# Performance work log

Hardware: AMD Instinct MI355X
Metric: run time of the kernel (lower is better)

## Reference

```python
import jax, jax.numpy as jnp
import numpy as np

VOCAB, E, H, L, B, OUT = 50000, 300, 300, 75, 2048, 5

def setup_inputs() -> dict:
    key = jax.random.key(0)
    ks = jax.random.split(key, 12)
    s_e = 1.0 / np.sqrt(E)
    s_h = 1.0 / np.sqrt(H)
    return {
        "input_sequences": jax.random.randint(ks[0], (B, L), 0, VOCAB),
        "emb": jax.random.normal(ks[1], (VOCAB, E), jnp.float32) * 0.1,
        "W_ih": jax.random.normal(ks[2], (3 * H, E), jnp.float32) * s_e,
        "W_hh": jax.random.normal(ks[3], (3 * H, H), jnp.float32) * s_h,
        "b_ih": jax.random.normal(ks[4], (3 * H,), jnp.float32) * s_h,
        "b_hh": jax.random.normal(ks[5], (3 * H,), jnp.float32) * s_h,
        "wCo_w": jax.random.normal(ks[6], (3 * H,), jnp.float32) * (1.0 / np.sqrt(3 * H)),
        "wCo_b": jax.random.normal(ks[7], (1,), jnp.float32) * 0.02,
        "Wmy_w": jax.random.normal(ks[8], (L,), jnp.float32) * (1.0 / np.sqrt(L)),
        "Wmy_b": jax.random.normal(ks[9], (1,), jnp.float32) * 0.02,
        "logits_w": jax.random.normal(ks[10], (OUT, H), jnp.float32) * s_h,
        "logits_b": jax.random.normal(ks[11], (OUT,), jnp.float32) * 0.02,
    }

def _gru(x_tm, W_ih, W_hh, b_ih, b_hh):
    # x_tm: (L, B, E) time-major. PyTorch GRU cell math.
    gx_all = jnp.einsum("lbe,ge->lbg", x_tm, W_ih) + b_ih  # (L, B, 3H)
    h0 = jnp.zeros((x_tm.shape[1], W_hh.shape[1]), x_tm.dtype)
    def step(h, gx):
        gh = h @ W_hh.T + b_hh
        xr, xz, xn = jnp.split(gx, 3, axis=-1)
        hr, hz, hn = jnp.split(gh, 3, axis=-1)
        r = jax.nn.sigmoid(xr + hr)
        z = jax.nn.sigmoid(xz + hz)
        n = jnp.tanh(xn + r * hn)
        h_new = (1.0 - z) * n + z * h
        return h_new, h_new
    _, ys = jax.lax.scan(step, h0, gx_all)
    return ys  # (L, B, H)

def reference(input_sequences, emb, W_ih, W_hh, b_ih, b_hh,
              wCo_w, wCo_b, Wmy_w, Wmy_b, logits_w, logits_b):
    x = emb[input_sequences]                      # (B, L, E)
    out_tm = _gru(x.transpose(1, 0, 2), W_ih, W_hh, b_ih, b_hh)  # (L, B, H)
    h = out_tm.transpose(1, 0, 2)                 # (B, L, H)
    # co_attention: s_ij = wCo @ cat(h_i, h_j, h_i*h_j) + b
    # computed WITHOUT materializing the (B, L, L, 3H) tensor:
    wa, wb, wc = jnp.split(wCo_w, 3)
    a = h @ wa                                    # (B, L)
    b = h @ wb                                    # (B, L)
    c = jnp.einsum("bid,bjd->bij", h * wc, h)     # (B, L, L)
    s = a[:, :, None] + b[:, None, :] + c + wCo_b[0]
    # zero the diagonal (mask = ones - diag)
    s = s * (1.0 - jnp.eye(s.shape[1], dtype=s.dtype))
    # Wmy: Linear(75, 1) over the j axis
    sm = s @ Wmy_w + Wmy_b[0]                     # (B, L)
    attn = jax.nn.softmax(sm, axis=1)             # softmax over i
    pooled = jnp.einsum("bi,bih->bh", attn, h)    # (B, H)
    return pooled @ logits_w.T + logits_b         # (B, OUT)
```

## Files before the change

kernel.cpp:

```cpp
#include <hip/hip_runtime.h>
#include <stdint.h>


typedef float f32x4 __attribute__((ext_vector_type(4)));
typedef short bf16x8 __attribute__((ext_vector_type(8)));
typedef _Float16 f16x4 __attribute__((ext_vector_type(4)));
typedef unsigned short u16;
typedef u16 u16x8 __attribute__((ext_vector_type(8)));
typedef u16 u16x4 __attribute__((ext_vector_type(4)));

#define DI __device__ __forceinline__

template <int N> struct IC { static constexpr int v = N; };

DI float bf2f(u16 v) {
    uint32_t u = ((uint32_t)v) << 16;
    float f;
    __builtin_memcpy(&f, &u, 4);
    return f;
}
DI u16 f2bf(float f) {
    uint32_t u;
    __builtin_memcpy(&u, &f, 4);
    uint32_t r = u + 0x7fffu + ((u >> 16) & 1u);
    return (u16)(r >> 16);
}
DI u16 cvt1(const void* p, int i, int f32m) {
    return f32m ? f2bf(((const float*)p)[i]) : ((const u16*)p)[i];
}

DI u16x8 load_row8(const u16* __restrict__ base, int e0) {
    u16x4 z = {0, 0, 0, 0};
    u16x4 lo = (e0 < 300) ? *(const u16x4*)(base + e0) : z;
    u16x4 hi = (e0 + 4 < 300) ? *(const u16x4*)(base + e0 + 4) : z;
    u16x8 r;
    r[0] = lo[0]; r[1] = lo[1]; r[2] = lo[2]; r[3] = lo[3];
    r[4] = hi[0]; r[5] = hi[1]; r[6] = hi[2]; r[7] = hi[3];
    return r;
}
DI u16x8 load_row8_f32(const float* __restrict__ base, int e0) {
    f32x4 z = {0.f, 0.f, 0.f, 0.f};
    f32x4 lo = (e0 < 300) ? *(const f32x4*)(base + e0) : z;
    f32x4 hi = (e0 + 4 < 300) ? *(const f32x4*)(base + e0 + 4) : z;
    u16x8 r;
    r[0] = f2bf(lo[0]); r[1] = f2bf(lo[1]); r[2] = f2bf(lo[2]); r[3] = f2bf(lo[3]);
    r[4] = f2bf(hi[0]); r[5] = f2bf(hi[1]); r[6] = f2bf(hi[2]); r[7] = f2bf(hi[3]);
    return r;
}

__global__ __launch_bounds__(256) void detect_dtype(const u16* __restrict__ raw,
                                                    int* __restrict__ flag) {
    __shared__ int cnt;
    if (threadIdx.x == 0) cnt = 0;
    __syncthreads();
    int local = 0;
    for (int i = threadIdx.x; i < 4096; i += 256) {
        int e = (raw[i] >> 7) & 0xFF;
        if (e >= 140) local++;
    }
    atomicAdd(&cnt, local);
    __syncthreads();
    if (threadIdx.x == 0) flag[0] = (cnt > 256) ? 1 : 0;
}

__global__ __launch_bounds__(256) void conv_big(const void* __restrict__ in,
                                                u16* __restrict__ outp, int n,
                                                const int* __restrict__ flag) {
    const int f32m = flag[0];
    int i0 = (blockIdx.x * 256 + threadIdx.x) * 8;
#pragma unroll
    for (int k = 0; k < 8; k++) {
        int i = i0 + k;
        if (i < n) outp[i] = cvt1(in, i, f32m);
    }
}

__global__ __launch_bounds__(256) void conv_smalls(
    const void* bih_r, const void* bhh_r, const void* wCo_r, const void* wCob_r,
    const void* Wmy_r, const void* Wmyb_r, const void* lw_r, const void* lb_r,
    u16* __restrict__ smalls, const int* __restrict__ flag) {
    const int f32m = flag[0];
    int t = blockIdx.x * 256 + threadIdx.x;
    if (t < 900) smalls[t] = cvt1(bih_r, t, f32m);
    else if (t < 1800) smalls[1024 + t - 900] = cvt1(bhh_r, t - 900, f32m);
    else if (t < 2700) smalls[2048 + t - 1800] = cvt1(wCo_r, t - 1800, f32m);
    else if (t < 2775) smalls[3072 + t - 2700] = cvt1(Wmy_r, t - 2700, f32m);
    else if (t < 4275) smalls[3200 + t - 2775] = cvt1(lw_r, t - 2775, f32m);
    else if (t < 4280) smalls[4704 + t - 4275] = cvt1(lb_r, t - 4275, f32m);
    else if (t == 4280) smalls[4712] = cvt1(wCob_r, 0, f32m);
    else if (t == 4281) smalls[4713] = cvt1(Wmyb_r, 0, f32m);
}

__global__ __launch_bounds__(256) void prep_img(const u16* __restrict__ W,
                                                u16* __restrict__ img) {
    int t = blockIdx.x * 256 + threadIdx.x;
    if (t >= 60 * 10 * 64) return;
    int lane = t & 63;
    int kt = (t >> 6) % 10;
    int nt = t / 640;
    int g = nt * 16 + (lane & 15);
    int gate = g / 320, u = g - gate * 320;
    int e0 = kt * 32 + (lane >> 4) * 8;
    u16x8 v;
    if (u < 300) {
        v = load_row8(W + (size_t)(gate * 300 + u) * 300, e0);
    } else {
        u16x8 z = {0, 0, 0, 0, 0, 0, 0, 0};
        v = z;
    }
    *(u16x8*)&img[(size_t)t * 8] = v;
}

__global__ __launch_bounds__(256) void zero_hstate(float* __restrict__ hs) {
    int t = blockIdx.x * 256 + threadIdx.x;
    f32x4 z = {0.f, 0.f, 0.f, 0.f};
    ((f32x4*)hs)[t] = z;
}

__global__ __launch_bounds__(256, 2) void gemm1_kernel(
    const int* __restrict__ seq, const void* __restrict__ emb_raw,
    const u16* __restrict__ Wimg, const u16* __restrict__ bih,
    _Float16* __restrict__ gxn, int ck, int phase, int BC, int bshift,
    const int* __restrict__ flag) {
    __shared__ int ids[192];
    __shared__ __align__(16) u16 Aimg[12 * 64 * 8];
    __shared__ __align__(16) u16 Bbuf[12 * 64 * 8];

    const int tid = threadIdx.x;
    const int lane = tid & 63, wv = tid >> 6, q = lane >> 4, c = lane & 15;
    const int m0 = blockIdx.x * 192;
    const int nb = blockIdx.y;
    const int f32m = flag[0];

    if (tid < 192) {
        int m = m0 + tid;
        int bc = m & (BC - 1);
        int tp = m >> bshift;
        ids[tid] = seq[(size_t)(phase * BC + bc) * 75 + ck * 15 + tp];
    }
    __syncthreads();

    f32x4 acc[3][12];
#pragma unroll
    for (int mt = 0; mt < 3; mt++)
#pragma unroll
        for (int nt = 0; nt < 12; nt++) {
            f32x4 z = {0.f, 0.f, 0.f, 0.f};
            acc[mt][nt] = z;
        }

    for (int kt = 0; kt < 10; kt++) {
#pragma unroll
        for (int s = 0; s < 3; s++) {
            int o = tid + s * 256;
            int qq = o / 192;
            int r = o - qq * 192;
            int e0 = kt * 32 + qq * 8;
            u16x8 v = f32m ? load_row8_f32((const float*)emb_raw + (size_t)ids[r] * 300, e0)
                           : load_row8((const u16*)emb_raw + (size_t)ids[r] * 300, e0);
            *(u16x8*)&Aimg[(((r >> 4) * 64) + ((r & 15) | (qq << 4))) * 8] = v;
        }
#pragma unroll
        for (int s = 0; s < 3; s++) {
            int ch = tid + s * 256;
            *(u16x8*)&Bbuf[ch * 8] =
                *(const u16x8*)&Wimg[(((size_t)(nb * 12 + (ch >> 6)) * 10 + kt) * 64 + (ch & 63)) * 8];
        }
        __syncthreads();

        bf16x8 a[3];
#pragma unroll
        for (int mt = 0; mt < 3; mt++) {
            u16x8 tmp = *(const u16x8*)&Aimg[(((wv * 3 + mt) * 64) + lane) * 8];
            a[mt] = __builtin_bit_cast(bf16x8, tmp);
        }
#pragma unroll
        for (int nt = 0; nt < 12; nt++) {
            u16x8 tb = *(const u16x8*)&Bbuf[(nt * 64 + lane) * 8];
            bf16x8 b = __builtin_bit_cast(bf16x8, tb);
#pragma unroll
            for (int mt = 0; mt < 3; mt++)
                acc[mt][nt] = __builtin_amdgcn_mfma_f32_16x16x32_bf16(a[mt], b, acc[mt][nt], 0, 0, 0);
        }
        __syncthreads();
    }

#pragma unroll
    for (int nt = 0; nt < 12; nt++) {
        int g = nb * 192 + nt * 16 + c;
        int gate = g / 320, u = g - gate * 320;
        float bias = (u < 300) ? bf2f(bih[gate * 300 + u]) : 0.f;
#pragma unroll
        for (int mt = 0; mt < 3; mt++) {
            int mrow = m0 + (wv * 3 + mt) * 16 + q * 4;
#pragma unroll
            for (int reg = 0; reg < 4; reg++) {
                gxn[((size_t)(mrow + reg) * 320 + u) * 4 + gate] =
                    (_Float16)(acc[mt][nt][reg] + bias);
            }
        }
    }
}

__global__ __launch_bounds__(512, 1) void gru_chunk(
    const _Float16* __restrict__ gxn, const u16* __restrict__ Wimg,
    const u16* __restrict__ bhh_g, u16* __restrict__ h_all,
    float* __restrict__ hstate, int ck, int BC) {
    __shared__ __align__(16) u16 Hhi[10 * 64 * 8];
    __shared__ __align__(16) u16 Hlo[10 * 64 * 8];
    __shared__ __align__(16) u16 Wlds[61440];

    const int tid = threadIdx.x;
    const int lane = tid & 63, wv = tid >> 6, q = lane >> 4, c = lane & 15;
    const int b0 = blockIdx.x * 16;
    const int wbase = (wv < 4) ? wv * 9216 : 36864 + (wv - 4) * 6144;

    float bhh[3][3];
    float hm[3][4];

    auto STAGE = [&](int kt, int buf, auto NTIC) {
        constexpr int NTI = NTIC.v;
        u16* dst = &Wlds[wbase + buf * (NTI * 3 * 512)];
#pragma unroll
        for (int Ti = 0; Ti < NTI; Ti++)
#pragma unroll
            for (int g = 0; g < 3; g++) {
                int nt = g * 20 + (wv + 8 * Ti);
                __builtin_amdgcn_global_load_lds(
                    (const unsigned int*)(Wimg + (size_t)(nt * 10 + kt) * 512 + lane * 8),
                    (unsigned int*)(dst + (Ti * 3 + g) * 512), 16, 0, 0);
            }
    };

    if (wv < 4) STAGE(0, 0, IC<3>{}); else STAGE(0, 0, IC<2>{});

    auto INIT = [&](auto NTIC) {
        constexpr int NTI = NTIC.v;
#pragma unroll
        for (int Ti = 0; Ti < NTI; Ti++) {
            int T = wv + 8 * Ti;
            int u = T * 16 + c;
#pragma unroll
            for (int g = 0; g < 3; g++)
                bhh[Ti][g] = (u < 300) ? bf2f(bhh_g[g * 300 + u]) : 0.f;
            int kti = T >> 1;
            int qp = ((T & 1) << 1) | (c >> 3);
            int j = c & 7;
#pragma unroll
            for (int reg = 0; reg < 4; reg++) {
                int m = q * 4 + reg;
                float h = hstate[(size_t)(b0 + m) * 320 + u];
                hm[Ti][reg] = h;
                int idx = (kti * 64 + ((q * 4 + reg) | (qp << 4))) * 8 + j;
                u16 hi = f2bf(h);
                Hhi[idx] = hi;
                Hlo[idx] = f2bf(h - bf2f(hi));
            }
        }
    };
    if (wv < 4) INIT(IC<3>{}); else INIT(IC<2>{});
    __syncthreads();

    for (int tt = 0; tt < 15; tt++) {
        auto PH1 = [&](auto NTIC) {
            constexpr int NTI = NTIC.v;
            constexpr int NT3 = NTI * 3;
            f16x4 gxv[NTI][4];
            const _Float16* gxt = gxn + (size_t)tt * BC * 1280;
#pragma unroll
            for (int Ti = 0; Ti < NTI; Ti++) {
                int u = (wv + 8 * Ti) * 16 + c;
#pragma unroll
                for (int reg = 0; reg < 4; reg++) {
                    int m = q * 4 + reg;
                    gxv[Ti][reg] = *(const f16x4*)&gxt[((size_t)(b0 + m) * 320 + u) * 4];
                }
            }

            f32x4 acc[NTI][3];
#pragma unroll
            for (int Ti = 0; Ti < NTI; Ti++)
#pragma unroll
                for (int g = 0; g < 3; g++) {
                    f32x4 z = {0.f, 0.f, 0.f, 0.f};
                    acc[Ti][g] = z;
                }

#pragma unroll 2
            for (int kt = 0; kt < 10; kt++) {
                if (kt < 9) STAGE(kt + 1, (kt + 1) & 1, NTIC);
                else if (tt < 14) STAGE(0, 0, NTIC);
                if (kt == 9 && tt == 14) {
                    asm volatile("s_waitcnt vmcnt(0)" ::: "memory");
                } else if constexpr (NTI == 3) {
                    asm volatile("s_waitcnt vmcnt(9)" ::: "memory");
                } else {
                    asm volatile("s_waitcnt vmcnt(6)" ::: "memory");
                }

                u16x8 th = *(const u16x8*)&Hhi[(kt * 64 + lane) * 8];
                u16x8 tl = *(const u16x8*)&Hlo[(kt * 64 + lane) * 8];
                bf16x8 ahi = __builtin_bit_cast(bf16x8, th);
                bf16x8 alo = __builtin_bit_cast(bf16x8, tl);
                const u16* wb = &Wlds[wbase + (kt & 1) * (NT3 * 512)];
#pragma unroll
                for (int Ti = 0; Ti < NTI; Ti++)
#pragma unroll
                    for (int g = 0; g < 3; g++) {
                        u16x8 tb = *(const u16x8*)&wb[(Ti * 3 + g) * 512 + lane * 8];
                        bf16x8 b = __builtin_bit_cast(bf16x8, tb);
                        acc[Ti][g] = __builtin_amdgcn_mfma_f32_16x16x32_bf16(
                            ahi, b, acc[Ti][g], 0, 0, 0);
                        acc[Ti][g] = __builtin_amdgcn_mfma_f32_16x16x32_bf16(
                            alo, b, acc[Ti][g], 0, 0, 0);
                    }
            }

            const int tglob = ck * 15 + tt;
#pragma unroll
            for (int Ti = 0; Ti < NTI; Ti++) {
                int u = (wv + 8 * Ti) * 16 + c;
#pragma unroll
                for (int reg = 0; reg < 4; reg++) {
                    int m = q * 4 + reg;
                    float xr = (float)gxv[Ti][reg][0];
                    float xz = (float)gxv[Ti][reg][1];
                    float xn = (float)gxv[Ti][reg][2];
                    float hr = acc[Ti][0][reg] + bhh[Ti][0];
                    float hz = acc[Ti][1][reg] + bhh[Ti][1];
                    float hn = acc[Ti][2][reg] + bhh[Ti][2];
                    float r = 1.f / (1.f + __expf(-(xr + hr)));
                    float z = 1.f / (1.f + __expf(-(xz + hz)));
                    float ex = __expf(2.f * (xn + r * hn));
                    float n = 1.f - 2.f / (ex + 1.f);
                    float h = (1.f - z) * n + z * hm[Ti][reg];
                    hm[Ti][reg] = h;
                    h_all[((size_t)tglob * BC + (b0 + m)) * 320 + u] = f2bf(h);
                }
            }
        };
        if (wv < 4) PH1(IC<3>{}); else PH1(IC<2>{});
        __syncthreads();

        auto FRAG = [&](auto NTIC) {
            constexpr int NTI = NTIC.v;
#pragma unroll
            for (int Ti = 0; Ti < NTI; Ti++) {
                int T = wv + 8 * Ti;
                int kti = T >> 1;
                int qp = ((T & 1) << 1) | (c >> 3);
                int j = c & 7;
#pragma unroll
                for (int reg = 0; reg < 4; reg++) {
                    int idx = (kti * 64 + ((q * 4 + reg) | (qp << 4))) * 8 + j;
                    float h = hm[Ti][reg];
                    u16 hi = f2bf(h);
                    Hhi[idx] = hi;
                    Hlo[idx] = f2bf(h - bf2f(hi));
                }
            }
        };
        if (wv < 4) FRAG(IC<3>{}); else FRAG(IC<2>{});
        __syncthreads();
    }

    auto PERSIST = [&](auto NTIC) {
        constexpr int NTI = NTIC.v;
#pragma unroll
        for (int Ti = 0; Ti < NTI; Ti++) {
            int u = (wv + 8 * Ti) * 16 + c;
#pragma unroll
            for (int reg = 0; reg < 4; reg++) {
                int m = q * 4 + reg;
                hstate[(size_t)(b0 + m) * 320 + u] = hm[Ti][reg];
            }
        }
    };
    if (wv < 4) PERSIST(IC<3>{}); else PERSIST(IC<2>{});
}

__global__ __launch_bounds__(256, 2) void coattn_kernel(
    const u16* __restrict__ h_all, const u16* __restrict__ smalls,
    void* __restrict__ outv, const int* __restrict__ flag, int phase, int BC) {
    __shared__ __align__(16) u16 himg[5 * 10 * 64 * 8];
    __shared__ float smacc[80], aArr[80], bArr[80], diagArr[80], attn[80], smv[80];
    __shared__ float pooled[320];
    __shared__ float scal[2];

    const u16* wCo = smalls + 2048;
    const u16* Wmy = smalls + 3072;
    const u16* lw = smalls + 3200;
    const u16* lb = smalls + 4704;
    const int f32out = flag[0];

    const int b = blockIdx.x;
    const int tid = threadIdx.x;
    const int lane = tid & 63, wv = tid >> 6, q = lane >> 4, c = lane & 15;

    for (int o = tid; o < 3200; o += 256) {
        int i = o / 40;
        int oc = o - i * 40;
        int kt = oc >> 2, qq = oc & 3;
        int e0 = kt * 32 + qq * 8;
        u16x8 v = {0, 0, 0, 0, 0, 0, 0, 0};
        if (i < 75) v = *(const u16x8*)(h_all + ((size_t)i * BC + b) * 320 + e0);
        *(u16x8*)&himg[(((i >> 4) * 10 + kt) * 64 + ((i & 15) | (qq << 4))) * 8] = v;
    }
    if (tid < 80) {
        smacc[tid] = 0.f; aArr[tid] = 0.f; bArr[tid] = 0.f;
        diagArr[tid] = 0.f; attn[tid] = 0.f;
    }
    __syncthreads();

    for (int pass = 0; pass < 2; pass++) {
        if (pass == 1 && wv != 0) break;
        int nt = (pass == 0) ? wv : 4;
        int jj = nt * 16 + c;
        bf16x8 bfr[10];
#pragma unroll
        for (int kt = 0; kt < 10; kt++) {
            int e0 = kt * 32 + q * 8;
            u16x8 res = {0, 0, 0, 0, 0, 0, 0, 0};
            if (jj < 75) {
                u16x8 hv = *(const u16x8*)&himg[((nt * 10 + kt) * 64 + lane) * 8];
                u16x8 wcv = load_row8(wCo + 600, e0);
#pragma unroll
                for (int j = 0; j < 8; j++) res[j] = f2bf(bf2f(hv[j]) * bf2f(wcv[j]));
            } else if (jj == 75) {
                res = load_row8(wCo, e0);
            } else if (jj == 76) {
                res = load_row8(wCo + 300, e0);
            }
            bfr[kt] = __builtin_bit_cast(bf16x8, res);
        }
        float wmyj = (jj < 75) ? bf2f(Wmy[jj]) : 0.f;

        for (int mt = 0; mt < 5; mt++) {
            f32x4 acc = {0.f, 0.f, 0.f, 0.f};
#pragma unroll
            for (int kt = 0; kt < 10; kt++) {
                u16x8 ta = *(const u16x8*)&himg[((mt * 10 + kt) * 64 + lane) * 8];
                bf16x8 a = __builtin_bit_cast(bf16x8, ta);
                acc = __builtin_amdgcn_mfma_f32_16x16x32_bf16(a, bfr[kt], acc, 0, 0, 0);
            }
#pragma unroll
            for (int reg = 0; reg < 4; reg++) {
                int i = mt * 16 + q * 4 + reg;
                float v = acc[reg];
                float p = v * wmyj;
                p += __shfl_xor(p, 1);
                p += __shfl_xor(p, 2);
                p += __shfl_xor(p, 4);
                p += __shfl_xor(p, 8);
                if (c == 0 && i < 75) atomicAdd(&smacc[i], p);
                if (jj == i && i < 75) diagArr[i] = v;
                if (jj == 75) aArr[i] = v;
                if (jj == 76) bArr[i] = v;
            }
        }
    }
    __syncthreads();

    if (tid < 64) {
        float w1 = bf2f(Wmy[tid]);
        float w2 = (tid + 64 < 75) ? bf2f(Wmy[tid + 64]) : 0.f;
        float s1 = w1 + w2;
        float s2 = w1 * bArr[tid] + ((tid + 64 < 75) ? w2 * bArr[tid + 64] : 0.f);
#pragma unroll
        for (int m = 1; m < 64; m <<= 1) {
            s1 += __shfl_xor(s1, m);
            s2 += __shfl_xor(s2, m);
        }
        if (tid == 0) { scal[0] = s1; scal[1] = s2; }
    }
    __syncthreads();

    float cb = bf2f(smalls[4712]);
    float wmyb = bf2f(smalls[4713]);
    if (tid < 75) {
        float Wi = bf2f(Wmy[tid]);
        smv[tid] = smacc[tid] - diagArr[tid] * Wi + (aArr[tid] + cb) * (scal[0] - Wi) +
                   scal[1] - bArr[tid] * Wi + wmyb;
    }
    __syncthreads();

    if (tid < 64) {
        float v1 = smv[tid];
        float v2 = (tid + 64 < 75) ? smv[tid + 64] : -1e30f;
        float mx = fmaxf(v1, v2);
#pragma unroll
        for (int m = 1; m < 64; m <<= 1) mx = fmaxf(mx, __shfl_xor(mx, m));
        float e1 = __expf(v1 - mx);
        float e2 = (tid + 64 < 75) ? __expf(v2 - mx) : 0.f;
        float s = e1 + e2;
#pragma unroll
        for (int m = 1; m < 64; m <<= 1) s += __shfl_xor(s, m);
        attn[tid] = e1 / s;
        if (tid + 64 < 75) attn[tid + 64] = e2 / s;
    }
    __syncthreads();

    for (int d = tid; d < 320; d += 256) {
        float accp = 0.f;
        for (int i = 0; i < 75; i++)
            accp += attn[i] * bf2f(h_all[((size_t)i * BC + b) * 320 + d]);
        pooled[d] = accp;
    }
    __syncthreads();

    if (tid < 160) {
        int o = tid >> 5, d0 = tid & 31;
        float accl = 0.f;
        for (int d = d0; d < 320; d += 32)
            accl += (d < 300) ? pooled[d] * bf2f(lw[o * 300 + d]) : 0.f;
#pragma unroll
        for (int m = 1; m < 32; m <<= 1) accl += __shfl_xor(accl, m);
        if (d0 == 0) {
            float v = accl + bf2f(lb[o]);
            size_t idx = (size_t)(phase * BC + b) * 5 + o;
            if (f32out) ((float*)outv)[idx] = v;
            else ((u16*)outv)[idx] = f2bf(v);
        }
    }
}

extern "C" void kernel_launch(void* const* d_in, const int* in_sizes, int n_in,
                              void* d_out, int out_size, void* d_ws, size_t ws_size,
                              hipStream_t stream) {
    const int* seq = (const int*)d_in[0];

    char* p = (char*)d_ws;
    int* flag = (int*)p;
    u16* smalls = (u16*)(p + 16);
    u16* WihImg = (u16*)(p + 9488);
    u16* WhhImg = (u16*)(p + 623888);
    u16* Wih_c = (u16*)(p + 1238288);
    u16* Whh_c = (u16*)(p + 1778288);
    const unsigned long long fixed_end = 2318288ull;

    auto req = [&](long long BC) -> unsigned long long {
        return fixed_end + (unsigned long long)BC * 87680ull + 1048576ull;
    };
    int BC = 256, bshift = 8;
    if (ws_size >= req(2048)) { BC = 2048; bshift = 11; }
    else if (ws_size >= req(1024)) { BC = 1024; bshift = 10; }
    else if (ws_size >= req(512)) { BC = 512; bshift = 9; }
    const int P = 2048 / BC;

    unsigned long long gx_b = 15ull * BC * 2560ull;
    unsigned long long h_b = 75ull * BC * 640ull;
    _Float16* gxn = (_Float16*)(p + fixed_end);
    u16* h_all = (u16*)(p + fixed_end + gx_b);
    float* hstate = (float*)(p + fixed_end + gx_b + h_b);

    detect_dtype<<<dim3(1), dim3(256), 0, stream>>>((const u16*)d_in[1], flag);
    conv_big<<<dim3((270000 + 2047) / 2048), dim3(256), 0, stream>>>(
        d_in[2], Wih_c, 270000, flag);
    conv_big<<<dim3((270000 + 2047) / 2048), dim3(256), 0, stream>>>(
        d_in[3], Whh_c, 270000, flag);
    conv_smalls<<<dim3(17), dim3(256), 0, stream>>>(
        d_in[4], d_in[5], d_in[6], d_in[7], d_in[8], d_in[9], d_in[10], d_in[11],
        smalls, flag);

    prep_img<<<dim3(150), dim3(256), 0, stream>>>(Wih_c, WihImg);
    prep_img<<<dim3(150), dim3(256), 0, stream>>>(Whh_c, WhhImg);

    for (int phase = 0; phase < P; phase++) {
        zero_hstate<<<dim3(BC * 320 / 1024), dim3(256), 0, stream>>>(hstate);
        for (int ck = 0; ck < 5; ck++) {
            gemm1_kernel<<<dim3(15 * BC / 192, 5), dim3(256), 0, stream>>>(
                seq, d_in[1], WihImg, smalls , gxn, ck, phase, BC, bshift, flag);
            gru_chunk<<<dim3(BC / 16), dim3(512), 0, stream>>>(
                gxn, WhhImg, smalls + 1024 , h_all, hstate, ck, BC);
        }
        coattn_kernel<<<dim3(BC), dim3(256), 0, stream>>>(h_all, smalls, d_out, flag,
                                                          phase, BC);
    }
}
```

Before: 1.517 ms.

## Swizzle coattn LDS layout, spread second pass across waves, pool from LDS

After: 1.458 ms. 1.04x faster.

```diff
diff --git a/kernel.cpp b/kernel.cpp
--- a/kernel.cpp
+++ b/kernel.cpp
@@ -379,13 +379,15 @@
     if (wv < 4) PERSIST(IC<3>{}); else PERSIST(IC<2>{});
 }
 
-__global__ __launch_bounds__(256, 2) void coattn_kernel(
+DI int hswz(int L, int kt) { return L ^ kt ^ (((L >> 4) & 3) << 1); }
+
+__global__ __launch_bounds__(256) void coattn_kernel(
     const u16* __restrict__ h_all, const u16* __restrict__ smalls,
     void* __restrict__ outv, const int* __restrict__ flag, int phase, int BC) {
     __shared__ __align__(16) u16 himg[5 * 10 * 64 * 8];
     __shared__ float smacc[80], aArr[80], bArr[80], diagArr[80], attn[80], smv[80];
-    __shared__ float pooled[320];
     __shared__ float scal[2];
+    __shared__ float logitsAcc[5];
 
     const u16* wCo = smalls + 2048;
     const u16* Wmy = smalls + 3072;
@@ -404,16 +406,16 @@
         int e0 = kt * 32 + qq * 8;
         u16x8 v = {0, 0, 0, 0, 0, 0, 0, 0};
         if (i < 75) v = *(const u16x8*)(h_all + ((size_t)i * BC + b) * 320 + e0);
-        *(u16x8*)&himg[(((i >> 4) * 10 + kt) * 64 + ((i & 15) | (qq << 4))) * 8] = v;
+        *(u16x8*)&himg[(((i >> 4) * 10 + kt) * 64 + hswz((i & 15) | (qq << 4), kt)) * 8] = v;
     }
     if (tid < 80) {
         smacc[tid] = 0.f; aArr[tid] = 0.f; bArr[tid] = 0.f;
         diagArr[tid] = 0.f; attn[tid] = 0.f;
     }
+    if (tid < 5) logitsAcc[tid] = 0.f;
     __syncthreads();
 
     for (int pass = 0; pass < 2; pass++) {
-        if (pass == 1 && wv != 0) break;
         int nt = (pass == 0) ? wv : 4;
         int jj = nt * 16 + c;
         bf16x8 bfr[10];
@@ -422,7 +424,7 @@
             int e0 = kt * 32 + q * 8;
             u16x8 res = {0, 0, 0, 0, 0, 0, 0, 0};
             if (jj < 75) {
-                u16x8 hv = *(const u16x8*)&himg[((nt * 10 + kt) * 64 + lane) * 8];
+                u16x8 hv = *(const u16x8*)&himg[((nt * 10 + kt) * 64 + hswz(lane, kt)) * 8];
                 u16x8 wcv = load_row8(wCo + 600, e0);
 #pragma unroll
                 for (int j = 0; j < 8; j++) res[j] = f2bf(bf2f(hv[j]) * bf2f(wcv[j]));
@@ -435,11 +437,13 @@
         }
         float wmyj = (jj < 75) ? bf2f(Wmy[jj]) : 0.f;
 
-        for (int mt = 0; mt < 5; mt++) {
+        int nmt = (pass == 0) ? 5 : (wv == 0 ? 2 : 1);
+        for (int mi = 0; mi < nmt; mi++) {
+            int mt = (pass == 0) ? mi : (wv == 0 ? mi * 4 : wv);
             f32x4 acc = {0.f, 0.f, 0.f, 0.f};
 #pragma unroll
             for (int kt = 0; kt < 10; kt++) {
-                u16x8 ta = *(const u16x8*)&himg[((mt * 10 + kt) * 64 + lane) * 8];
+                u16x8 ta = *(const u16x8*)&himg[((mt * 10 + kt) * 64 + hswz(lane, kt)) * 8];
                 bf16x8 a = __builtin_bit_cast(bf16x8, ta);
                 acc = __builtin_amdgcn_mfma_f32_16x16x32_bf16(a, bfr[kt], acc, 0, 0, 0);
             }
@@ -500,27 +504,34 @@
     }
     __syncthreads();
 
-    for (int d = tid; d < 320; d += 256) {
-        float accp = 0.f;
-        for (int i = 0; i < 75; i++)
-            accp += attn[i] * bf2f(h_all[((size_t)i * BC + b) * 320 + d]);
-        pooled[d] = accp;
-    }
-    __syncthreads();
-
-    if (tid < 160) {
-        int o = tid >> 5, d0 = tid & 31;
-        float accl = 0.f;
-        for (int d = d0; d < 320; d += 32)
-            accl += (d < 300) ? pooled[d] * bf2f(lw[o * 300 + d]) : 0.f;
-#pragma unroll
-        for (int m = 1; m < 32; m <<= 1) accl += __shfl_xor(accl, m);
-        if (d0 == 0) {
-            float v = accl + bf2f(lb[o]);
-            size_t idx = (size_t)(phase * BC + b) * 5 + o;
-            if (f32out) ((float*)outv)[idx] = v;
-            else ((u16*)outv)[idx] = f2bf(v);
-        }
+    const int d1 = tid, d2 = tid + 256;
+    float pd1 = 0.f, pd2 = 0.f;
+    {
+        const int kt1 = d1 >> 5, qq1 = (d1 >> 3) & 3, j1 = d1 & 7;
+        const int kt2 = d2 >> 5, qq2 = (d2 >> 3) & 3, j2 = d2 & 7;
+        for (int i = 0; i < 75; i++) {
+            float a = attn[i];
+            int ih = i >> 4, il = i & 15;
+            pd1 += a * bf2f(himg[((ih * 10 + kt1) * 64 + hswz(il | (qq1 << 4), kt1)) * 8 + j1]);
+            if (wv == 0)
+                pd2 += a * bf2f(himg[((ih * 10 + kt2) * 64 + hswz(il | (qq2 << 4), kt2)) * 8 + j2]);
+        }
+    }
+#pragma unroll
+    for (int o = 0; o < 5; o++) {
+        float part = (d1 < 300) ? pd1 * bf2f(lw[o * 300 + d1]) : 0.f;
+        if (wv == 0 && d2 < 300) part += pd2 * bf2f(lw[o * 300 + d2]);
+#pragma unroll
+        for (int m = 1; m < 64; m <<= 1) part += __shfl_xor(part, m);
+        if (lane == 0) atomicAdd(&logitsAcc[o], part);
+    }
+    __syncthreads();
+
+    if (tid < 5) {
+        float v = logitsAcc[tid] + bf2f(lb[tid]);
+        size_t idx = (size_t)(phase * BC + b) * 5 + tid;
+        if (f32out) ((float*)outv)[idx] = v;
+        else ((u16*)outv)[idx] = f2bf(v);
     }
 }
 
```
